# Kernel optimization log

Measured on AMD Instinct MI355X. Metric: run time of the kernel, lower is better.

Reference implementation:

```python
import jax, jax.numpy as jnp
import numpy as np
import math

N, B, T, E = 4, 8, 2, 1024
H, D = 16, 64
S, L = 2048, 1024
NB = N * B

def setup_inputs() -> dict:
    key = jax.random.key(0)
    ks = jax.random.split(key, 10)
    sc = 0.02
    return {
        'hidden_states': jax.random.normal(ks[0], (NB, T, E), jnp.float32),
        'attention_mask': jnp.zeros((NB, 1, 1, S + L + T), jnp.float32),
        'past_prefix_key': jax.random.normal(ks[1], (N, H, S, D), jnp.float32),
        'past_prefix_value': jax.random.normal(ks[2], (N, H, S, D), jnp.float32),
        'past_key': jax.random.normal(ks[3], (NB, H, L, D), jnp.float32),
        'past_value': jax.random.normal(ks[4], (NB, H, L, D), jnp.float32),
        'Wq': jax.random.normal(ks[5], (E, E), jnp.float32) * sc,
        'bq': jnp.zeros((E,), jnp.float32),
        'Wk': jax.random.normal(ks[6], (E, E), jnp.float32) * sc,
        'bk': jnp.zeros((E,), jnp.float32),
        'Wv': jax.random.normal(ks[7], (E, E), jnp.float32) * sc,
        'bv': jnp.zeros((E,), jnp.float32),
    }

def _heads(x):
    # (NB, T, E) -> (NB, H, T, D)
    return x.reshape(NB, T, H, D).transpose(0, 2, 1, 3)

def reference(hidden_states, attention_mask, past_prefix_key, past_prefix_value,
              past_key, past_value, Wq, bq, Wk, bk, Wv, bv):
    scale = 1.0 / math.sqrt(D)
    q = _heads(hidden_states @ Wq.T + bq)   # (NB,H,T,D)
    k_new = _heads(hidden_states @ Wk.T + bk)
    v_new = _heads(hidden_states @ Wv.T + bv)

    # prefix scores: broadcast shared prefix KV across beams
    q_beam = q.reshape(N, B, H, T, D)
    prefix_scores = jnp.einsum('bxhtd,bhsd->bxhts', q_beam, past_prefix_key)
    prefix_scores = prefix_scores.reshape(NB, H, T, S) * scale

    # current KV = cached target prefix + new tokens
    k = jnp.concatenate([past_key, k_new], axis=2)   # (NB,H,L+T,D)
    v = jnp.concatenate([past_value, v_new], axis=2)
    cur_scores = jnp.einsum('bhtd,bhsd->bhts', q, k) * scale

    scores = jnp.concatenate([prefix_scores, cur_scores], axis=-1) + attention_mask
    probs = jax.nn.softmax(scores, axis=-1)          # (NB,H,T,S+L+T)

    prefix_probs = probs[..., :S].reshape(N, B, H, T, S)
    cur_probs = probs[..., S:]
    prefix_ctx = jnp.einsum('bxhts,bhsd->bxhtd', prefix_probs, past_prefix_value)
    prefix_ctx = prefix_ctx.reshape(NB, H, T, D)
    ctx = prefix_ctx + jnp.einsum('bhts,bhsd->bhtd', cur_probs, v)

    # (NB,H,T,D) -> (NB,T,E)
    return ctx.transpose(0, 2, 1, 3).reshape(NB, T, H * D)
```

## Files before the change

### kernel.cpp

```cpp
#include <hip/hip_runtime.h>
#include <hip/hip_bf16.h>

#define NB_  32
#define T_   2
#define E_   1024
#define H_   16
#define D_   64
#define S_   2048
#define L_   1024
#define TOT_ (S_ + L_ + T_)

#define PCH_  16
#define PLEN_ (S_ / PCH_)
#define CCH_  8
#define CLEN_ (L_ / CCH_)

#define PFXBLK_ (4 * H_ * PCH_)
#define CURBLK_ (NB_ * H_ * CCH_)

#define LOG2E_ 1.4426950408889634f
#define QS_ (0.125f * LOG2E_)

__global__ __launch_bounds__(256) void qkv_kernel(
    const float* __restrict__ hidden,
    const float* __restrict__ Wq, const float* __restrict__ bq,
    const float* __restrict__ Wk, const float* __restrict__ bk,
    const float* __restrict__ Wv, const float* __restrict__ bv,
    float* __restrict__ qT,
    float* __restrict__ knew,
    float* __restrict__ vnew)
{
    __shared__ float ldsT[128 * 65];
    __shared__ float wlds[16 * 128];
    const int tid  = threadIdx.x;
    const int wave = tid >> 6;
    const int lane = tid & 63;
    const int eg0  = blockIdx.x * 16;
    const int mat  = eg0 >> 10;
    const int e0   = eg0 & 1023;
    int c0 = wave * 4;
    c0 = __builtin_amdgcn_readfirstlane(c0);

    const float* W    = (mat == 0) ? Wq : (mat == 1) ? Wk : Wv;
    const float* bias = (mat == 0) ? bq : (mat == 1) ? bk : bv;

    float acc[4] = {0.f, 0.f, 0.f, 0.f};

    for (int k0 = 0; k0 < 1024; k0 += 128) {
        __syncthreads();
        #pragma unroll
        for (int i = 0; i < 32; i++) {
            int f = i * 256 + tid;
            int r = f >> 7;
            int c = f & 127;
            ldsT[c * 65 + r] = hidden[r * 1024 + k0 + c];
        }
        #pragma unroll
        for (int i = 0; i < 2; i++) {
            int wr = (tid >> 5) + i * 8;
            int wc = (tid & 31) * 4;
            *reinterpret_cast<float4*>(&wlds[wr * 128 + wc]) =
                *reinterpret_cast<const float4*>(&W[(size_t)(e0 + wr) * 1024 + k0 + wc]);
        }
        __syncthreads();

        for (int kk = 0; kk < 128; kk += 4) {
            float h0 = ldsT[(kk + 0) * 65 + lane];
            float h1 = ldsT[(kk + 1) * 65 + lane];
            float h2 = ldsT[(kk + 2) * 65 + lane];
            float h3 = ldsT[(kk + 3) * 65 + lane];
            float4 w0 = *reinterpret_cast<const float4*>(&wlds[(c0 + 0) * 128 + kk]);
            float4 w1 = *reinterpret_cast<const float4*>(&wlds[(c0 + 1) * 128 + kk]);
            float4 w2 = *reinterpret_cast<const float4*>(&wlds[(c0 + 2) * 128 + kk]);
            float4 w3 = *reinterpret_cast<const float4*>(&wlds[(c0 + 3) * 128 + kk]);
            acc[0] = fmaf(h0, w0.x, acc[0]); acc[0] = fmaf(h1, w0.y, acc[0]);
            acc[0] = fmaf(h2, w0.z, acc[0]); acc[0] = fmaf(h3, w0.w, acc[0]);
            acc[1] = fmaf(h0, w1.x, acc[1]); acc[1] = fmaf(h1, w1.y, acc[1]);
            acc[1] = fmaf(h2, w1.z, acc[1]); acc[1] = fmaf(h3, w1.w, acc[1]);
            acc[2] = fmaf(h0, w2.x, acc[2]); acc[2] = fmaf(h1, w2.y, acc[2]);
            acc[2] = fmaf(h2, w2.z, acc[2]); acc[2] = fmaf(h3, w2.w, acc[2]);
            acc[3] = fmaf(h0, w3.x, acc[3]); acc[3] = fmaf(h1, w3.y, acc[3]);
            acc[3] = fmaf(h2, w3.z, acc[3]); acc[3] = fmaf(h3, w3.w, acc[3]);
        }
    }

    const int r = lane;
    #pragma unroll
    for (int j = 0; j < 4; j++) {
        int e_in = e0 + c0 + j;
        float val = acc[j] + bias[e_in];
        if (mat == 0) {
            qT[e_in * 64 + r] = val;
        } else {
            int nb = r >> 1, t = r & 1, h = e_in >> 6, d = e_in & 63;
            float* dst = (mat == 1) ? knew : vnew;
            dst[((nb * H_ + h) * T_ + t) * D_ + d] = val;
        }
    }
}

__global__ __launch_bounds__(256) void partial_kernel(
    const float* __restrict__ mask,
    const float* __restrict__ pfx_k,
    const float* __restrict__ pfx_v,
    const float* __restrict__ pk,
    const float* __restrict__ pv,
    const float* __restrict__ qT,
    const float* __restrict__ knew,
    const float* __restrict__ vnew,
    float* __restrict__ cur_ctx,
    float* __restrict__ cur_l,
    float* __restrict__ pfx_ctx,
    float* __restrict__ pfx_l)
{
    __shared__ float sred[4160];
    const int tid = threadIdx.x;

    if (blockIdx.x < PFXBLK_) {
        const int idx   = blockIdx.x;
        const int n     = idx >> 8;
        const int h     = (idx >> 4) & 15;
        const int chunk = idx & 15;
        const int wv    = tid >> 6;
        const int lane  = tid & 63;
        const int r     = lane & 15;
        const int c     = lane >> 4;

        float qreg[16];
        const float* qbase = qT + (h * 64 + c * 16) * 64 + (n * 16 + r);
        #pragma unroll
        for (int u = 0; u < 16; u++) qreg[u] = qbase[u * 64] * QS_;

        const size_t pos0 = (size_t)(n * H_ + h) * S_ + chunk * PLEN_;
        const float* kb = pfx_k + pos0 * D_ + c * 16;
        const float* vb = pfx_v + pos0 * D_ + c * 16;
        const float* mrow = mask + (n * 8 + (r >> 1)) * TOT_ + chunk * PLEN_;

        float ctx[16];
        #pragma unroll
        for (int u = 0; u < 16; u++) ctx[u] = 0.f;
        float lsum = 0.f;

        #pragma unroll 2
        for (int i = 0; i < PLEN_ / 4; i++) {
            int p = i * 4 + wv;
            const float* kp = kb + p * D_;
            float4 k0 = *reinterpret_cast<const float4*>(kp + 0);
            float4 k1 = *reinterpret_cast<const float4*>(kp + 4);
            float4 k2 = *reinterpret_cast<const float4*>(kp + 8);
            float4 k3 = *reinterpret_cast<const float4*>(kp + 12);
            float sA = qreg[0]*k0.x;  sA = fmaf(qreg[1],k0.y,sA);
            sA = fmaf(qreg[2],k0.z,sA); sA = fmaf(qreg[3],k0.w,sA);
            float sB = qreg[4]*k1.x;  sB = fmaf(qreg[5],k1.y,sB);
            sB = fmaf(qreg[6],k1.z,sB); sB = fmaf(qreg[7],k1.w,sB);
            float sC = qreg[8]*k2.x;  sC = fmaf(qreg[9],k2.y,sC);
            sC = fmaf(qreg[10],k2.z,sC); sC = fmaf(qreg[11],k2.w,sC);
            float sD = qreg[12]*k3.x; sD = fmaf(qreg[13],k3.y,sD);
            sD = fmaf(qreg[14],k3.z,sD); sD = fmaf(qreg[15],k3.w,sD);
            float s = (sA + sB) + (sC + sD);
            s += __shfl_xor(s, 16, 64);
            s += __shfl_xor(s, 32, 64);
            float e = exp2f(s + mrow[p] * LOG2E_);
            lsum += e;
            const float* vp = vb + p * D_;
            float4 v0 = *reinterpret_cast<const float4*>(vp + 0);
            float4 v1 = *reinterpret_cast<const float4*>(vp + 4);
            float4 v2 = *reinterpret_cast<const float4*>(vp + 8);
            float4 v3 = *reinterpret_cast<const float4*>(vp + 12);
            ctx[0]  += e * v0.x; ctx[1]  += e * v0.y; ctx[2]  += e * v0.z; ctx[3]  += e * v0.w;
            ctx[4]  += e * v1.x; ctx[5]  += e * v1.y; ctx[6]  += e * v1.z; ctx[7]  += e * v1.w;
            ctx[8]  += e * v2.x; ctx[9]  += e * v2.y; ctx[10] += e * v2.z; ctx[11] += e * v2.w;
            ctx[12] += e * v3.x; ctx[13] += e * v3.y; ctx[14] += e * v3.z; ctx[15] += e * v3.w;
        }

        const int base = wv * 1024 + r * 64 + c * 16;
        #pragma unroll
        for (int u = 0; u < 16; u += 4)
            *reinterpret_cast<float4*>(&sred[base + u]) =
                make_float4(ctx[u], ctx[u+1], ctx[u+2], ctx[u+3]);
        if (c == 0) sred[4096 + wv * 16 + r] = lsum;
        __syncthreads();

        const int pc = (n * H_ + h) * PCH_ + chunk;
        for (int e = tid; e < 1024; e += 256) {
            float s = sred[e] + sred[1024 + e] + sred[2048 + e] + sred[3072 + e];
            pfx_ctx[pc * 1024 + e] = s;
        }
        if (tid < 16) {
            float l = sred[4096 + tid] + sred[4096 + 16 + tid]
                    + sred[4096 + 32 + tid] + sred[4096 + 48 + tid];
            pfx_l[pc * 16 + tid] = l;
        }
    } else {
        const int idx   = blockIdx.x - PFXBLK_;
        const int b     = idx >> 3;
        const int chunk = idx & 7;
        const int nb    = b >> 4;
        const int h     = b & 15;
        const int g     = tid >> 4;
        const int l16   = tid & 15;
        const int d0    = l16 * 4;

        float qf0[4], qf1[4];
        #pragma unroll
        for (int j = 0; j < 4; j++) {
            const float* qb = qT + (h * 64 + d0 + j) * 64 + nb * 2;
            qf0[j] = qb[0] * QS_;
            qf1[j] = qb[1] * QS_;
        }

        const float* pk_b = pk + ((nb * H_ + h) * (size_t)L_) * D_;
        const float* pv_b = pv + ((nb * H_ + h) * (size_t)L_) * D_;
        const float* mrow = mask + nb * TOT_ + S_;

        float l0 = 0.f, l1 = 0.f;
        float a0[4] = {0.f,0.f,0.f,0.f};
        float a1[4] = {0.f,0.f,0.f,0.f};

        const int p0 = chunk * CLEN_ + g;
        #pragma unroll 2
        for (int i = 0; i < CLEN_ / 16; i++) {
            int p = p0 + i * 16;
            float4 kf = *reinterpret_cast<const float4*>(pk_b + p * D_ + d0);
            float s0 = fmaf(qf0[0],kf.x, qf0[1]*kf.y) + fmaf(qf0[2],kf.z, qf0[3]*kf.w);
            float s1 = fmaf(qf1[0],kf.x, qf1[1]*kf.y) + fmaf(qf1[2],kf.z, qf1[3]*kf.w);
            #pragma unroll
            for (int off = 1; off < 16; off <<= 1) {
                s0 += __shfl_xor(s0, off, 64);
                s1 += __shfl_xor(s1, off, 64);
            }
            float mC = mrow[p] * LOG2E_;
            float e0 = exp2f(s0 + mC);
            float e1 = exp2f(s1 + mC);
            l0 += e0; l1 += e1;
            float4 vf = *reinterpret_cast<const float4*>(pv_b + p * D_ + d0);
            a0[0] += e0 * vf.x; a0[1] += e0 * vf.y; a0[2] += e0 * vf.z; a0[3] += e0 * vf.w;
            a1[0] += e1 * vf.x; a1[1] += e1 * vf.y; a1[2] += e1 * vf.z; a1[3] += e1 * vf.w;
        }
        if (chunk == 7 && g < 2) {
            const float* kn_b = knew + (nb * H_ + h) * (T_ * D_);
            const float* vn_b = vnew + (nb * H_ + h) * (T_ * D_);
            float4 kf = *reinterpret_cast<const float4*>(kn_b + g * D_ + d0);
            float s0 = fmaf(qf0[0],kf.x, qf0[1]*kf.y) + fmaf(qf0[2],kf.z, qf0[3]*kf.w);
            float s1 = fmaf(qf1[0],kf.x, qf1[1]*kf.y) + fmaf(qf1[2],kf.z, qf1[3]*kf.w);
            #pragma unroll
            for (int off = 1; off < 16; off <<= 1) {
                s0 += __shfl_xor(s0, off, 64);
                s1 += __shfl_xor(s1, off, 64);
            }
            float mC = mrow[L_ + g] * LOG2E_;
            float e0 = exp2f(s0 + mC);
            float e1 = exp2f(s1 + mC);
            l0 += e0; l1 += e1;
            float4 vf = *reinterpret_cast<const float4*>(vn_b + g * D_ + d0);
            a0[0] += e0 * vf.x; a0[1] += e0 * vf.y; a0[2] += e0 * vf.z; a0[3] += e0 * vf.w;
            a1[0] += e1 * vf.x; a1[1] += e1 * vf.y; a1[2] += e1 * vf.z; a1[3] += e1 * vf.w;
        }

        #pragma unroll
        for (int j = 0; j < 4; j++) {
            sred[g * 128 + d0 + j]      = a0[j];
            sred[g * 128 + 64 + d0 + j] = a1[j];
        }
        if (l16 == 0) { sred[2048 + g * 2] = l0; sred[2048 + g * 2 + 1] = l1; }
        __syncthreads();

        if (tid < 128) {
            int t = tid >> 6, d = tid & 63;
            float s = 0.f, l = 0.f;
            for (int g2 = 0; g2 < 16; g2++) {
                s += sred[g2 * 128 + t * 64 + d];
                l += sred[2048 + g2 * 2 + t];
            }
            const int cb = b * CCH_ + chunk;
            cur_ctx[(cb * 2 + t) * 64 + d] = s;
            if (d == 0) cur_l[cb * 2 + t] = l;
        }
    }
}

__global__ __launch_bounds__(1024) void combine_kernel(
    const float* __restrict__ cur_ctx, const float* __restrict__ cur_l,
    const float* __restrict__ pfx_ctx, const float* __restrict__ pfx_l,
    float* __restrict__ out)
{
    const int row = blockIdx.x;
    const int nb  = row >> 1, t = row & 1;
    const int n   = nb >> 3;
    const int r   = (nb & 7) * 2 + t;
    const int tid = threadIdx.x;
    const int h   = tid >> 6, d = tid & 63;
    const int b   = nb * 16 + h;

    float val = 0.f, l = 0.f;
    #pragma unroll
    for (int ch = 0; ch < CCH_; ch++) {
        int cb = b * CCH_ + ch;
        val += cur_ctx[(cb * 2 + t) * 64 + d];
        l   += cur_l[cb * 2 + t];
    }
    #pragma unroll
    for (int ch = 0; ch < PCH_; ch++) {
        int pc = (n * H_ + h) * PCH_ + ch;
        val += pfx_ctx[pc * 1024 + r * 64 + d];
        l   += pfx_l[pc * 16 + r];
    }
    out[row * 1024 + tid] = val / l;
}

extern "C" void kernel_launch(void* const* d_in, const int* in_sizes, int n_in,
                              void* d_out, int out_size, void* d_ws, size_t ws_size,
                              hipStream_t stream) {
    const float* hidden = (const float*)d_in[0];
    const float* mask   = (const float*)d_in[1];
    const float* pfxk   = (const float*)d_in[2];
    const float* pfxv   = (const float*)d_in[3];
    const float* pk     = (const float*)d_in[4];
    const float* pv     = (const float*)d_in[5];
    const float* Wq     = (const float*)d_in[6];
    const float* bq     = (const float*)d_in[7];
    const float* Wk     = (const float*)d_in[8];
    const float* bk     = (const float*)d_in[9];
    const float* Wv     = (const float*)d_in[10];
    const float* bv     = (const float*)d_in[11];

    float* qT      = (float*)d_ws;
    float* knew    = qT + 65536;
    float* vnew    = knew + 65536;
    float* cur_ctx = vnew + 65536;
    float* cur_l   = cur_ctx + 524288;
    float* pfx_ctx = cur_l + 8192;
    float* pfx_l   = pfx_ctx + 1048576;

    qkv_kernel<<<192, 256, 0, stream>>>(hidden, Wq, bq, Wk, bk, Wv, bv,
                                        qT, knew, vnew);
    partial_kernel<<<PFXBLK_ + CURBLK_, 256, 0, stream>>>(
        mask, pfxk, pfxv, pk, pv, qT, knew, vnew,
        cur_ctx, cur_l, pfx_ctx, pfx_l);
    combine_kernel<<<64, 1024, 0, stream>>>(cur_ctx, cur_l, pfx_ctx, pfx_l,
                                            (float*)d_out);
}
```

Measured before the change: 128.6 us.

## Rebalance attention partial kernel so every block does prefix and cached work

```diff
diff --git a/kernel.cpp b/kernel.cpp
--- a/kernel.cpp
+++ b/kernel.cpp
@@ -10,13 +10,14 @@
 #define L_   1024
 #define TOT_ (S_ + L_ + T_)
 
-#define PCH_  16
+#define PCH_  32
 #define PLEN_ (S_ / PCH_)
 #define CCH_  8
 #define CLEN_ (L_ / CCH_)
 
-#define PFXBLK_ (4 * H_ * PCH_)
-#define CURBLK_ (NB_ * H_ * CCH_)
+#define PFXU_ (4 * H_ * PCH_)
+#define CURU_ (NB_ * H_ * CCH_)
+#define GRID_ 2048
 
 #define LOG2E_ 1.4426950408889634f
 #define QS_ (0.125f * LOG2E_)
@@ -99,7 +100,7 @@
     }
 }
 
-__global__ __launch_bounds__(256) void partial_kernel(
+__global__ __launch_bounds__(256, 8) void partial_kernel(
     const float* __restrict__ mask,
     const float* __restrict__ pfx_k,
     const float* __restrict__ pfx_v,
@@ -116,11 +117,11 @@
     __shared__ float sred[4160];
     const int tid = threadIdx.x;
 
-    if (blockIdx.x < PFXBLK_) {
-        const int idx   = blockIdx.x;
-        const int n     = idx >> 8;
-        const int h     = (idx >> 4) & 15;
-        const int chunk = idx & 15;
+    {
+        const int v     = blockIdx.x;
+        const int n     = v >> 9;
+        const int h     = (v >> 5) & 15;
+        const int chunk = v & 31;
         const int wv    = tid >> 6;
         const int lane  = tid & 63;
         const int r     = lane & 15;
@@ -191,10 +192,14 @@
                     + sred[4096 + 32 + tid] + sred[4096 + 48 + tid];
             pfx_l[pc * 16 + tid] = l;
         }
-    } else {
-        const int idx   = blockIdx.x - PFXBLK_;
-        const int b     = idx >> 3;
-        const int chunk = idx & 7;
+    }
+
+    #pragma unroll 1
+    for (int kph = 0; kph < 2; kph++) {
+        __syncthreads();
+        const int u     = blockIdx.x + kph * GRID_;
+        const int b     = u >> 3;
+        const int chunk = u & 7;
         const int nb    = b >> 4;
         const int h     = b & 15;
         const int g     = tid >> 4;
@@ -218,10 +223,19 @@
         float a1[4] = {0.f,0.f,0.f,0.f};
 
         const int p0 = chunk * CLEN_ + g;
-        #pragma unroll 2
-        for (int i = 0; i < CLEN_ / 16; i++) {
-            int p = p0 + i * 16;
-            float4 kf = *reinterpret_cast<const float4*>(pk_b + p * D_ + d0);
+        float4 kf = *reinterpret_cast<const float4*>(pk_b + (size_t)p0 * D_ + d0);
+        float4 vf = *reinterpret_cast<const float4*>(pv_b + (size_t)p0 * D_ + d0);
+        float  mv = mrow[p0];
+
+        #pragma unroll
+        for (int i = 0; i < 8; i++) {
+            float4 kf2, vf2; float m2;
+            if (i < 7) {
+                int pn = p0 + (i + 1) * 16;
+                kf2 = *reinterpret_cast<const float4*>(pk_b + (size_t)pn * D_ + d0);
+                vf2 = *reinterpret_cast<const float4*>(pv_b + (size_t)pn * D_ + d0);
+                m2  = mrow[pn];
+            }
             float s0 = fmaf(qf0[0],kf.x, qf0[1]*kf.y) + fmaf(qf0[2],kf.z, qf0[3]*kf.w);
             float s1 = fmaf(qf1[0],kf.x, qf1[1]*kf.y) + fmaf(qf1[2],kf.z, qf1[3]*kf.w);
             #pragma unroll
@@ -229,20 +243,21 @@
                 s0 += __shfl_xor(s0, off, 64);
                 s1 += __shfl_xor(s1, off, 64);
             }
-            float mC = mrow[p] * LOG2E_;
+            float mC = mv * LOG2E_;
             float e0 = exp2f(s0 + mC);
             float e1 = exp2f(s1 + mC);
             l0 += e0; l1 += e1;
-            float4 vf = *reinterpret_cast<const float4*>(pv_b + p * D_ + d0);
             a0[0] += e0 * vf.x; a0[1] += e0 * vf.y; a0[2] += e0 * vf.z; a0[3] += e0 * vf.w;
             a1[0] += e1 * vf.x; a1[1] += e1 * vf.y; a1[2] += e1 * vf.z; a1[3] += e1 * vf.w;
-        }
+            if (i < 7) { kf = kf2; vf = vf2; mv = m2; }
+        }
+
         if (chunk == 7 && g < 2) {
             const float* kn_b = knew + (nb * H_ + h) * (T_ * D_);
             const float* vn_b = vnew + (nb * H_ + h) * (T_ * D_);
-            float4 kf = *reinterpret_cast<const float4*>(kn_b + g * D_ + d0);
-            float s0 = fmaf(qf0[0],kf.x, qf0[1]*kf.y) + fmaf(qf0[2],kf.z, qf0[3]*kf.w);
-            float s1 = fmaf(qf1[0],kf.x, qf1[1]*kf.y) + fmaf(qf1[2],kf.z, qf1[3]*kf.w);
+            float4 kfn = *reinterpret_cast<const float4*>(kn_b + g * D_ + d0);
+            float s0 = fmaf(qf0[0],kfn.x, qf0[1]*kfn.y) + fmaf(qf0[2],kfn.z, qf0[3]*kfn.w);
+            float s1 = fmaf(qf1[0],kfn.x, qf1[1]*kfn.y) + fmaf(qf1[2],kfn.z, qf1[3]*kfn.w);
             #pragma unroll
             for (int off = 1; off < 16; off <<= 1) {
                 s0 += __shfl_xor(s0, off, 64);
@@ -252,9 +267,9 @@
             float e0 = exp2f(s0 + mC);
             float e1 = exp2f(s1 + mC);
             l0 += e0; l1 += e1;
-            float4 vf = *reinterpret_cast<const float4*>(vn_b + g * D_ + d0);
-            a0[0] += e0 * vf.x; a0[1] += e0 * vf.y; a0[2] += e0 * vf.z; a0[3] += e0 * vf.w;
-            a1[0] += e1 * vf.x; a1[1] += e1 * vf.y; a1[2] += e1 * vf.z; a1[3] += e1 * vf.w;
+            float4 vfn = *reinterpret_cast<const float4*>(vn_b + g * D_ + d0);
+            a0[0] += e0 * vfn.x; a0[1] += e0 * vfn.y; a0[2] += e0 * vfn.z; a0[3] += e0 * vfn.w;
+            a1[0] += e1 * vfn.x; a1[1] += e1 * vfn.y; a1[2] += e1 * vfn.z; a1[3] += e1 * vfn.w;
         }
 
         #pragma unroll
@@ -272,30 +287,30 @@
                 s += sred[g2 * 128 + t * 64 + d];
                 l += sred[2048 + g2 * 2 + t];
             }
-            const int cb = b * CCH_ + chunk;
-            cur_ctx[(cb * 2 + t) * 64 + d] = s;
-            if (d == 0) cur_l[cb * 2 + t] = l;
+            cur_ctx[(u * 2 + t) * 64 + d] = s;
+            if (d == 0) cur_l[u * 2 + t] = l;
         }
     }
 }
 
-__global__ __launch_bounds__(1024) void combine_kernel(
+__global__ __launch_bounds__(256) void combine_kernel(
     const float* __restrict__ cur_ctx, const float* __restrict__ cur_l,
     const float* __restrict__ pfx_ctx, const float* __restrict__ pfx_l,
     float* __restrict__ out)
 {
-    const int row = blockIdx.x;
+    const int row = blockIdx.x >> 2;
+    const int qtr = blockIdx.x & 3;
     const int nb  = row >> 1, t = row & 1;
     const int n   = nb >> 3;
     const int r   = (nb & 7) * 2 + t;
-    const int tid = threadIdx.x;
-    const int h   = tid >> 6, d = tid & 63;
+    const int e   = qtr * 256 + threadIdx.x;
+    const int h   = e >> 6, d = e & 63;
     const int b   = nb * 16 + h;
 
     float val = 0.f, l = 0.f;
     #pragma unroll
     for (int ch = 0; ch < CCH_; ch++) {
-        int cb = b * CCH_ + ch;
+        int cb = (b * CCH_ + ch);
         val += cur_ctx[(cb * 2 + t) * 64 + d];
         l   += cur_l[cb * 2 + t];
     }
@@ -305,7 +320,7 @@
         val += pfx_ctx[pc * 1024 + r * 64 + d];
         l   += pfx_l[pc * 16 + r];
     }
-    out[row * 1024 + tid] = val / l;
+    out[row * 1024 + e] = val / l;
 }
 
 extern "C" void kernel_launch(void* const* d_in, const int* in_sizes, int n_in,
@@ -330,13 +345,13 @@
     float* cur_ctx = vnew + 65536;
     float* cur_l   = cur_ctx + 524288;
     float* pfx_ctx = cur_l + 8192;
-    float* pfx_l   = pfx_ctx + 1048576;
+    float* pfx_l   = pfx_ctx + 2097152;
 
     qkv_kernel<<<192, 256, 0, stream>>>(hidden, Wq, bq, Wk, bk, Wv, bv,
                                         qT, knew, vnew);
-    partial_kernel<<<PFXBLK_ + CURBLK_, 256, 0, stream>>>(
+    partial_kernel<<<GRID_, 256, 0, stream>>>(
         mask, pfxk, pfxv, pk, pv, qT, knew, vnew,
         cur_ctx, cur_l, pfx_ctx, pfx_l);
-    combine_kernel<<<64, 1024, 0, stream>>>(cur_ctx, cur_l, pfx_ctx, pfx_l,
+    combine_kernel<<<256, 256, 0, stream>>>(cur_ctx, cur_l, pfx_ctx, pfx_l,
                                             (float*)d_out);
 }
```

Result: slower. 194.2 us (+51.0%).
